# Kernel tuning notes

Hardware: AMD Instinct MI355X
Metric: run time of the kernel (lower is better)

Reference implementation:

```python
import jax, jax.numpy as jnp
import numpy as np

N_NODES = 100000
N_EDGES = 1600000
IN_FEAT = 128
UNITS = 64


def setup_inputs() -> dict:
    key = jax.random.key(0)
    k1, k2, k3, k4, k5 = jax.random.split(key, 5)
    node_states = jax.random.normal(k1, (N_NODES, IN_FEAT), dtype=jnp.float32)
    # edges[:,0] is the destination/segment id; the original TF code's
    # repeat(bincount) normalization assumes edges sorted by edges[:,0].
    dst = jnp.sort(jax.random.randint(k2, (N_EDGES,), 0, N_NODES))
    src = jax.random.randint(k3, (N_EDGES,), 0, N_NODES)
    edges = jnp.stack([dst, src], axis=1).astype(jnp.int64)
    kernel = jax.random.normal(k4, (IN_FEAT, UNITS), dtype=jnp.float32) * 0.05
    kernel_attention = jax.random.normal(k5, (2 * UNITS, 1), dtype=jnp.float32) * 0.05
    return {"node_states": node_states, "edges": edges,
            "kernel": kernel, "kernel_attention": kernel_attention}


def reference(node_states, edges, kernel, kernel_attention):
    n_nodes = node_states.shape[0]
    dst = edges[:, 0]  # segment ids (aggregation target)
    src = edges[:, 1]  # neighbor being gathered

    h = node_states @ kernel                      # [N, U]
    h_dst = h[dst]                                # [E, U]
    h_src = h[src]                                # [E, U]
    # concat(h_dst, h_src) @ a  ==  h_dst @ a[:U] + h_src @ a[U:]
    u = kernel_attention.shape[0] // 2
    scores = (h_dst @ kernel_attention[:u] + h_src @ kernel_attention[u:])[:, 0]  # [E]
    scores = jax.nn.leaky_relu(scores, negative_slope=0.2)  # tf default alpha=0.2
    scores = jnp.exp(jnp.clip(scores, -2.0, 2.0))

    score_sum = jax.ops.segment_sum(scores, dst, num_segments=n_nodes)  # [N]
    attn = scores / score_sum[dst]                                      # [E]

    out = jax.ops.segment_sum(h_src * attn[:, None], dst, num_segments=n_nodes)  # [N, U]
    return out
```

## Files before the change

kernel.cpp:

```cpp
#include <hip/hip_runtime.h>
#include <hip/hip_bf16.h>

#define NN 100000
#define NE 1600000
#define NF 128
#define UU 64

typedef __attribute__((ext_vector_type(8))) short short8;
typedef __attribute__((ext_vector_type(4))) float f32x4;

static const size_t OFF_FLAG = 0;
static const size_t OFF_H2   = 256;
static const size_t OFF_AD   = OFF_H2  + (size_t)NN * UU * 2;
static const size_t OFF_AS   = OFF_AD  + (size_t)NN * 4;
static const size_t OFF_ROW  = OFF_AS  + (size_t)NN * 4;
static const size_t OFF_WP   = OFF_ROW + (size_t)(NN + 1) * 4;

__device__ __forceinline__ unsigned short bfr(float v) {
    unsigned u = __float_as_uint(v);
    return (unsigned short)((u + 0x7FFFu + ((u >> 16) & 1u)) >> 16);
}

__global__ __launch_bounds__(256) void prep(const int* __restrict__ ew,
                                            const float* __restrict__ W,
                                            int* __restrict__ flag,
                                            unsigned short* __restrict__ Wp) {
    if (blockIdx.x == 0) {
        if (threadIdx.x == 0) {
            int a = ew[2 * 400000 + 1] | ew[2 * 800000 + 1] |
                    ew[2 * 1200000 + 1] | ew[2 * 1599999 + 1];
            *flag = (a == 0) ? 1 : 0;
        }
        return;
    }
    int i = (blockIdx.x - 1) * 256 + threadIdx.x;
    int j   = i & 7;
    int l15 = (i >> 3) & 15;
    int quad = (i >> 7) & 3;
    int kb  = (i >> 9) & 3;
    int nt  = i >> 11;
    Wp[i] = bfr(W[(size_t)(kb * 32 + quad * 8 + j) * UU + nt * 16 + l15]);
}

#define GEMM_BLOCKS   1563
#define ROWS_BLOCKS   391

__global__ __launch_bounds__(256) void mega(const float* __restrict__ X,
                                            const void* __restrict__ edges,
                                            const int* __restrict__ flag,
                                            const unsigned short* __restrict__ Wp,
                                            const float* __restrict__ ka,
                                            unsigned short* __restrict__ h2,
                                            float* __restrict__ a_dst,
                                            float* __restrict__ a_src,
                                            int* __restrict__ rows) {
    int bid = blockIdx.x;
    int tid = threadIdx.x;

    if (bid < GEMM_BLOCKS) {
        int wv = tid >> 6, lane = tid & 63;
        int quad = lane >> 4, l15 = lane & 15;
        int nb = bid * 64 + wv * 16;
        int row = nb + l15; if (row >= NN) row = NN - 1;
        const float* xr = X + (size_t)row * NF + quad * 8;

        short8 afrag[4];
#pragma unroll
        for (int kb = 0; kb < 4; kb++) {
            float4 p0 = *(const float4*)(xr + kb * 32);
            float4 p1 = *(const float4*)(xr + kb * 32 + 4);
            short8 a;
            a[0] = (short)bfr(p0.x); a[1] = (short)bfr(p0.y);
            a[2] = (short)bfr(p0.z); a[3] = (short)bfr(p0.w);
            a[4] = (short)bfr(p1.x); a[5] = (short)bfr(p1.y);
            a[6] = (short)bfr(p1.z); a[7] = (short)bfr(p1.w);
            afrag[kb] = a;
        }

        f32x4 acc[4] = {f32x4{0,0,0,0}, f32x4{0,0,0,0}, f32x4{0,0,0,0}, f32x4{0,0,0,0}};
        const short8* wpf = (const short8*)Wp;
#pragma unroll
        for (int nt = 0; nt < 4; nt++) {
#pragma unroll
            for (int kb = 0; kb < 4; kb++) {
                short8 b = wpf[((nt * 4 + kb) * 4 + quad) * 16 + l15];
                acc[nt] = __builtin_amdgcn_mfma_f32_16x16x32_bf16(afrag[kb], b, acc[nt], 0, 0, 0);
            }
        }

        float kad[4], kas[4];
#pragma unroll
        for (int nt = 0; nt < 4; nt++) {
            kad[nt] = ka[nt * 16 + l15];
            kas[nt] = ka[64 + nt * 16 + l15];
        }
#pragma unroll
        for (int r = 0; r < 4; r++) {
            int m = nb + quad * 4 + r;
            if (m < NN) {
#pragma unroll
                for (int nt = 0; nt < 4; nt++)
                    h2[(size_t)m * UU + nt * 16 + l15] = bfr(acc[nt][r]);
            }
            float pd = acc[0][r] * kad[0] + acc[1][r] * kad[1] + acc[2][r] * kad[2] + acc[3][r] * kad[3];
            float ps = acc[0][r] * kas[0] + acc[1][r] * kas[1] + acc[2][r] * kas[2] + acc[3][r] * kas[3];
            pd += __shfl_xor(pd, 1); pd += __shfl_xor(pd, 2);
            pd += __shfl_xor(pd, 4); pd += __shfl_xor(pd, 8);
            ps += __shfl_xor(ps, 1); ps += __shfl_xor(ps, 2);
            ps += __shfl_xor(ps, 4); ps += __shfl_xor(ps, 8);
            if (l15 == 0 && m < NN) { a_dst[m] = pd; a_src[m] = ps; }
        }
        return;
    }
    bid -= GEMM_BLOCKS;

    {
        int n = bid * 256 + tid;
        if (n > NN) return;
        if (n == NN) { rows[NN] = NE; return; }
        int fl = *flag;
        const int* ew = (const int*)edges;
        int lo = 0, hi = NE;
        while (lo < hi) {
            int mid = (lo + hi) >> 1;
            int d = fl ? ew[4 * (size_t)mid] : ew[2 * (size_t)mid];
            if (d < n) lo = mid + 1; else hi = mid;
        }
        rows[n] = lo;
    }
}

__device__ __forceinline__ float edge_score(float ad, float as) {
    float sc = ad + as;
    sc = sc > 0.f ? sc : 0.2f * sc;
    sc = fminf(fmaxf(sc, -2.f), 2.f);
    return __expf(sc);
}

__global__ __launch_bounds__(256) void aggregate(const void* __restrict__ edges,
                                                 const int* __restrict__ flag,
                                                 const int* __restrict__ rows,
                                                 const float* __restrict__ a_dst,
                                                 const float* __restrict__ a_src,
                                                 const unsigned short* __restrict__ h2,
                                                 float* __restrict__ out) {
    int tid = threadIdx.x;
    int lane = tid & 63;
    int g = lane >> 4, gl = lane & 15;
    int n = blockIdx.x * 16 + (tid >> 6) * 4 + g;
    if (n >= NN) return;
    int s = rows[n], e = rows[n + 1];
    int cnt = e - s;
    float ad = a_dst[n];
    int fl = *flag;
    const int* ew = (const int*)edges;
    const int* sp = ew + (fl ? 2 : 1);
    int lsh = fl ? 2 : 1;
    const unsigned short* h2g = h2 + gl * 4;
    int gbase = g * 16;
    float4 acc = make_float4(0.f, 0.f, 0.f, 0.f);
    float inv;

#define BATCH(MS, MW, BOFF)                                                  \
    {                                                                        \
        uint2 rr[4]; float sw[4]; int sjv[4];                                \
        _Pragma("unroll")                                                    \
        for (int t = 0; t < 4; t++) {                                        \
            sjv[t] = __shfl(MS, gbase + (BOFF) + t);                         \
            sw[t]  = __shfl(MW, gbase + (BOFF) + t);                         \
        }                                                                    \
        _Pragma("unroll")                                                    \
        for (int t = 0; t < 4; t++)                                          \
            rr[t] = *(const uint2*)(h2g + (size_t)sjv[t] * UU);              \
        _Pragma("unroll")                                                    \
        for (int t = 0; t < 4; t++) {                                        \
            acc.x += sw[t] * __uint_as_float(rr[t].x << 16);                 \
            acc.y += sw[t] * __uint_as_float(rr[t].x & 0xFFFF0000u);         \
            acc.z += sw[t] * __uint_as_float(rr[t].y << 16);                 \
            acc.w += sw[t] * __uint_as_float(rr[t].y & 0xFFFF0000u);         \
        }                                                                    \
    }

    if (cnt <= 64) {
        int msrc[4]; float mw[4];
#pragma unroll
        for (int k = 0; k < 4; k++) {
            int c = k * 16 + gl;
            int sj = 0; float w = 0.f;
            if (c < cnt) {
                sj = sp[(size_t)(s + c) << lsh];
                w = edge_score(ad, a_src[sj]);
            }
            msrc[k] = sj; mw[k] = w;
        }
        float t0 = (mw[0] + mw[1]) + (mw[2] + mw[3]);
        t0 += __shfl_xor(t0, 1); t0 += __shfl_xor(t0, 2);
        t0 += __shfl_xor(t0, 4); t0 += __shfl_xor(t0, 8);
        inv = (cnt > 0) ? 1.f / t0 : 0.f;
#pragma unroll
        for (int k = 0; k < 4; k++) {
#pragma unroll
            for (int b = 0; b < 4; b++) {
                if (k * 16 + b * 4 < cnt) BATCH(msrc[k], mw[k], b * 4);
            }
        }
    } else {
        float t0 = 0.f;
        for (int c = gl; c < cnt; c += 16) {
            int sj = sp[(size_t)(s + c) << lsh];
            t0 += edge_score(ad, a_src[sj]);
        }
        t0 += __shfl_xor(t0, 1); t0 += __shfl_xor(t0, 2);
        t0 += __shfl_xor(t0, 4); t0 += __shfl_xor(t0, 8);
        inv = 1.f / t0;
        for (int c0 = 0; c0 < cnt; c0 += 16) {
            int c = c0 + gl;
            int sj = 0; float w = 0.f;
            if (c < cnt) {
                sj = sp[(size_t)(s + c) << lsh];
                w = edge_score(ad, a_src[sj]);
            }
#pragma unroll
            for (int b = 0; b < 4; b++) {
                if (c0 + b * 4 < cnt) BATCH(sj, w, b * 4);
            }
        }
    }
#undef BATCH

    float4 o;
    o.x = acc.x * inv; o.y = acc.y * inv;
    o.z = acc.z * inv; o.w = acc.w * inv;
    *(float4*)(out + (size_t)n * UU + gl * 4) = o;
}

extern "C" void kernel_launch(void* const* d_in, const int* in_sizes, int n_in,
                              void* d_out, int out_size, void* d_ws, size_t ws_size,
                              hipStream_t stream) {
    const float* X  = (const float*)d_in[0];
    const void*  Ed = d_in[1];
    const float* W  = (const float*)d_in[2];
    const float* KA = (const float*)d_in[3];
    float* out = (float*)d_out;

    char* ws = (char*)d_ws;
    int*            flag  = (int*)(ws + OFF_FLAG);
    unsigned short* h2    = (unsigned short*)(ws + OFF_H2);
    float*          a_dst = (float*)(ws + OFF_AD);
    float*          a_src = (float*)(ws + OFF_AS);
    int*            rows  = (int*)(ws + OFF_ROW);
    unsigned short* Wp    = (unsigned short*)(ws + OFF_WP);

    prep<<<33, 256, 0, stream>>>((const int*)Ed, W, flag, Wp);
    mega<<<GEMM_BLOCKS + ROWS_BLOCKS, 256, 0, stream>>>(
        X, Ed, flag, Wp, KA, h2, a_dst, a_src, rows);
    aggregate<<<NN / 16, 256, 0, stream>>>(Ed, flag, rows, a_dst, a_src, h2, out);
}
```

Before: 145.2 us.

## Issue first gather batch before score loads and use packed bf16 conversion

The short-segment aggregation path now loads source indices, then issues the first 16 h2 row gathers before fetching a_src and computing edge scores. This overlaps gather latency with the dependent score loads. The normalisation sum is moved after accumulation. Separately, the manual round-to-nearest bf16 conversion in the GEMM is replaced with the v_cvt_pk_bf16_f32 instruction, which packs two values per instruction, at the cost of more live registers for the prefetched rows.

```diff
diff --git a/kernel.cpp b/kernel.cpp
--- a/kernel.cpp
+++ b/kernel.cpp
@@ -8,6 +8,7 @@
 
 typedef __attribute__((ext_vector_type(8))) short short8;
 typedef __attribute__((ext_vector_type(4))) float f32x4;
+typedef __attribute__((ext_vector_type(4))) unsigned u32x4;
 
 static const size_t OFF_FLAG = 0;
 static const size_t OFF_H2   = 256;
@@ -19,6 +20,12 @@
 __device__ __forceinline__ unsigned short bfr(float v) {
     unsigned u = __float_as_uint(v);
     return (unsigned short)((u + 0x7FFFu + ((u >> 16) & 1u)) >> 16);
+}
+
+__device__ __forceinline__ unsigned cvtpk(float lo, float hi) {
+    unsigned r;
+    asm("v_cvt_pk_bf16_f32 %0, %1, %2" : "=v"(r) : "v"(lo), "v"(hi));
+    return r;
 }
 
 __global__ __launch_bounds__(256) void prep(const int* __restrict__ ew,
@@ -69,12 +76,10 @@
         for (int kb = 0; kb < 4; kb++) {
             float4 p0 = *(const float4*)(xr + kb * 32);
             float4 p1 = *(const float4*)(xr + kb * 32 + 4);
-            short8 a;
-            a[0] = (short)bfr(p0.x); a[1] = (short)bfr(p0.y);
-            a[2] = (short)bfr(p0.z); a[3] = (short)bfr(p0.w);
-            a[4] = (short)bfr(p1.x); a[5] = (short)bfr(p1.y);
-            a[6] = (short)bfr(p1.z); a[7] = (short)bfr(p1.w);
-            afrag[kb] = a;
+            u32x4 aw;
+            aw[0] = cvtpk(p0.x, p0.y); aw[1] = cvtpk(p0.z, p0.w);
+            aw[2] = cvtpk(p1.x, p1.y); aw[3] = cvtpk(p1.z, p1.w);
+            afrag[kb] = __builtin_bit_cast(short8, aw);
         }
 
         f32x4 acc[4] = {f32x4{0,0,0,0}, f32x4{0,0,0,0}, f32x4{0,0,0,0}, f32x4{0,0,0,0}};
@@ -99,8 +104,10 @@
             int m = nb + quad * 4 + r;
             if (m < NN) {
 #pragma unroll
-                for (int nt = 0; nt < 4; nt++)
-                    h2[(size_t)m * UU + nt * 16 + l15] = bfr(acc[nt][r]);
+                for (int nt = 0; nt < 4; nt++) {
+                    unsigned v = cvtpk(acc[nt][r], acc[nt][r]);
+                    h2[(size_t)m * UU + nt * 16 + l15] = (unsigned short)v;
+                }
             }
             float pd = acc[0][r] * kad[0] + acc[1][r] * kad[1] + acc[2][r] * kad[2] + acc[3][r] * kad[3];
             float ps = acc[0][r] * kas[0] + acc[1][r] * kas[1] + acc[2][r] * kas[2] + acc[3][r] * kas[3];
@@ -182,28 +189,57 @@
     }
 
     if (cnt <= 64) {
-        int msrc[4]; float mw[4];
+        int msrc[4];
 #pragma unroll
         for (int k = 0; k < 4; k++) {
             int c = k * 16 + gl;
-            int sj = 0; float w = 0.f;
-            if (c < cnt) {
-                sj = sp[(size_t)(s + c) << lsh];
-                w = edge_score(ad, a_src[sj]);
-            }
-            msrc[k] = sj; mw[k] = w;
+            msrc[k] = (c < cnt) ? sp[(size_t)(s + c) << lsh] : 0;
+        }
+        int sjv0[4][4];
+#pragma unroll
+        for (int b = 0; b < 4; b++)
+#pragma unroll
+            for (int t = 0; t < 4; t++)
+                sjv0[b][t] = __shfl(msrc[0], gbase + b * 4 + t);
+        uint2 rr0[4][4];
+#pragma unroll
+        for (int b = 0; b < 4; b++) {
+            if (b * 4 < cnt) {
+#pragma unroll
+                for (int t = 0; t < 4; t++)
+                    rr0[b][t] = *(const uint2*)(h2g + (size_t)sjv0[b][t] * UU);
+            }
+        }
+        float mw[4];
+#pragma unroll
+        for (int k = 0; k < 4; k++) {
+            int c = k * 16 + gl;
+            mw[k] = (c < cnt) ? edge_score(ad, a_src[msrc[k]]) : 0.f;
+        }
+#pragma unroll
+        for (int b = 0; b < 4; b++) {
+            if (b * 4 < cnt) {
+#pragma unroll
+                for (int t = 0; t < 4; t++) {
+                    float w = __shfl(mw[0], gbase + b * 4 + t);
+                    acc.x += w * __uint_as_float(rr0[b][t].x << 16);
+                    acc.y += w * __uint_as_float(rr0[b][t].x & 0xFFFF0000u);
+                    acc.z += w * __uint_as_float(rr0[b][t].y << 16);
+                    acc.w += w * __uint_as_float(rr0[b][t].y & 0xFFFF0000u);
+                }
+            }
+        }
+#pragma unroll
+        for (int k = 1; k < 4; k++) {
+#pragma unroll
+            for (int b = 0; b < 4; b++) {
+                if (k * 16 + b * 4 < cnt) BATCH(msrc[k], mw[k], b * 4);
+            }
         }
         float t0 = (mw[0] + mw[1]) + (mw[2] + mw[3]);
         t0 += __shfl_xor(t0, 1); t0 += __shfl_xor(t0, 2);
         t0 += __shfl_xor(t0, 4); t0 += __shfl_xor(t0, 8);
         inv = (cnt > 0) ? 1.f / t0 : 0.f;
-#pragma unroll
-        for (int k = 0; k < 4; k++) {
-#pragma unroll
-            for (int b = 0; b < 4; b++) {
-                if (k * 16 + b * 4 < cnt) BATCH(msrc[k], mw[k], b * 4);
-            }
-        }
     } else {
         float t0 = 0.f;
         for (int c = gl; c < cnt; c += 16) {
```

New measurement: 145.6 us. About the same (+0.3%).
